# Kernel optimization log

Measured on AMD Instinct MI355X. Metric: run time of the kernel, lower is better.

## Reference

```python
import jax, jax.numpy as jnp
import numpy as np

V, E, H, T, B, D, L = 32000, 512, 512, 128, 4, 4, 2
C0, C1 = 2000, 10000          # adaptive softmax cutoffs
NT = T - D + 1


def setup_inputs() -> dict:
    key = jax.random.key(0)
    ks = jax.random.split(key, 18)
    s = 0.02
    x = jax.random.randint(ks[0], (B, T), 1, V)
    lengths = jnp.sort(jax.random.randint(ks[1], (B,), D, T + 1))[::-1]
    lengths = lengths.at[0].set(T)
    # graph predictor output: per-layer attention matrices [B, L, T, T]
    G = jax.nn.softmax(jax.random.normal(ks[2], (B, L, T, T)), axis=-1)
    emb = (jax.random.normal(ks[3], (V, E)) * s).at[0].set(0.0)  # padding_idx=0
    enc_w_ih = jax.random.normal(ks[4], (L, 3 * H, H)) * s
    enc_w_hh = jax.random.normal(ks[5], (L, 3 * H, H)) * s
    enc_b_ih = jnp.zeros((L, 3 * H))
    enc_b_hh = jnp.zeros((L, 3 * H))
    dec_w_ih = jax.random.normal(ks[6], (3 * H, E)) * s
    dec_w_hh = jax.random.normal(ks[7], (3 * H, H)) * s
    dec_b_ih = jnp.zeros((3 * H,))
    dec_b_hh = jnp.zeros((3 * H,))
    head_w = jax.random.normal(ks[8], (C0 + 2, H)) * s
    t0_proj = jax.random.normal(ks[9], (H // 4, H)) * s
    t0_out = jax.random.normal(ks[10], (C1 - C0, H // 4)) * s
    t1_proj = jax.random.normal(ks[11], (H // 16, H)) * s
    t1_out = jax.random.normal(ks[12], (V - C1, H // 16)) * s
    return dict(x=x, lengths=lengths, G=G, emb=emb,
                enc_w_ih=enc_w_ih, enc_w_hh=enc_w_hh, enc_b_ih=enc_b_ih, enc_b_hh=enc_b_hh,
                dec_w_ih=dec_w_ih, dec_w_hh=dec_w_hh, dec_b_ih=dec_b_ih, dec_b_hh=dec_b_hh,
                head_w=head_w, t0_proj=t0_proj, t0_out=t0_out, t1_proj=t1_proj, t1_out=t1_out)


def gru_step(xt, h, w_ih, w_hh, b_ih, b_hh):
    """torch nn.GRU/GRUCell math; works on arbitrary leading dims."""
    gi = xt @ w_ih.T + b_ih
    gh = h @ w_hh.T + b_hh
    i_r, i_z, i_n = jnp.split(gi, 3, axis=-1)
    h_r, h_z, h_n = jnp.split(gh, 3, axis=-1)
    r = jax.nn.sigmoid(i_r + h_r)
    z = jax.nn.sigmoid(i_z + h_z)
    n = jnp.tanh(i_n + r * h_n)
    return (1.0 - z) * n + z * h


def adaptive_log_prob(h, head_w, t0_proj, t0_out, t1_proj, t1_out):
    """torch AdaptiveLogSoftmaxWithLoss.log_prob: h [N,H] -> [N,V]."""
    head_lp = jax.nn.log_softmax(h @ head_w.T, axis=-1)                      # [N, C0+2]
    lp0 = head_lp[:, C0:C0 + 1] + jax.nn.log_softmax((h @ t0_proj.T) @ t0_out.T, axis=-1)
    lp1 = head_lp[:, C0 + 1:C0 + 2] + jax.nn.log_softmax((h @ t1_proj.T) @ t1_out.T, axis=-1)
    return jnp.concatenate([head_lp[:, :C0], lp0, lp1], axis=-1)


def reference(x, lengths, G, emb, enc_w_ih, enc_w_hh, enc_b_ih, enc_b_hh,
              dec_w_ih, dec_w_hh, dec_b_ih, dec_b_hh,
              head_w, t0_proj, t0_out, t1_proj, t1_out):
    b = x.shape[0]
    input_f = emb[x]                      # [B,T,E] (dropout p=0)
    embedded = input_f
    # ---- encoder: graph-weighted aggregation + GRUCell per layer ----
    for l in range(enc_w_ih.shape[0]):
        wgt = jnp.einsum('bji,bjd->bid', G[:, l], input_f)   # G_l^T @ input_f
        input_f = gru_step(wgt, input_f, enc_w_ih[l], enc_w_hh[l], enc_b_ih[l], enc_b_hh[l])
    # ---- decoder: length-D GRU window per start position t ----
    t_idx = jnp.arange(NT)
    d_idx = jnp.arange(D)
    tok_idx = jnp.broadcast_to(t_idx[None, :, None] + d_idx[None, None, :] - 1, (b, NT, D))
    tok_idx = tok_idx.at[:, 0, 0].set(lengths - 1)           # t=0,d=0 uses embedded[lengths-1]
    wins = jnp.take_along_axis(embedded, tok_idx.reshape(b, -1)[:, :, None], axis=1)
    wins = wins.reshape(b, NT, D, E)
    h0 = input_f[:, :NT, :]                                  # [B,NT,H]
    def step(h, xd):
        hn = gru_step(xd, h, dec_w_ih, dec_w_hh, dec_b_ih, dec_b_hh)
        return hn, hn
    _, hs = jax.lax.scan(step, h0, jnp.moveaxis(wins, 2, 0))  # [D,B,NT,H]
    hs = jnp.moveaxis(hs, 0, 2)                               # [B,NT,D,H]
    # pad_packed_sequence zeros hidden beyond per-row lens = min(lengths - t, D)
    valid = (t_idx[None, :, None] + d_idx[None, None, :]) < lengths[:, None, None]
    hs = jnp.where(valid[..., None], hs, 0.0)
    lp = adaptive_log_prob(hs.reshape(-1, H), head_w, t0_proj, t0_out, t1_proj, t1_out)
    lp = lp.reshape(b, NT, D, V)
    # batch rows with lengths <= t were excluded and F.pad'ed with zeros
    row_valid = t_idx[None, :] < lengths[:, None]
    lp = jnp.where(row_valid[:, :, None, None], lp, 0.0)
    return lp.reshape(b, NT * D, V)
```

## Files before the change

kernel.cpp:

```cpp
#include <hip/hip_runtime.h>
#include <hip/hip_bf16.h>
#include <hip/hip_fp16.h>

typedef __hip_bfloat16 bf16;
typedef __attribute__((ext_vector_type(8))) short short8v;
typedef __attribute__((ext_vector_type(4))) float float4v;

#define V_    32000
#define E_    512
#define H_    512
#define T_    128
#define B_    4
#define D_    4
#define L_    2
#define C0_   2000
#define C1_   10000
#define NT_   125
#define NROW_ 2000
#define NH_   2002
#define NTOTC 2162
#define NSLOT 252

__device__ __forceinline__ float bf2f(bf16 v) { return __bfloat162float(v); }
__device__ __forceinline__ unsigned short f2bfu(float f) {
    bf16 h = __float2bfloat16(f);
    union { bf16 h; unsigned short u; } cv; cv.h = h; return cv.u;
}
__device__ __forceinline__ float ld1(const void* p, size_t i, int bf) {
    return bf ? bf2f(((const bf16*)p)[i]) : ((const float*)p)[i];
}

__device__ __forceinline__ void lse_push(float z, float& m, float& s) {
    if (z <= m) { s += __expf(z - m); }
    else        { s = s * __expf(m - z) + 1.0f; m = z; }
}
__device__ __forceinline__ void lse_merge(float m2, float s2, float& m, float& s) {
    float mm = fmaxf(m, m2);
    s = s * __expf(m - mm) + s2 * __expf(m2 - mm);
    m = mm;
}

__global__ void k_detect(const void* __restrict__ G, int* __restrict__ flag) {
    int t = threadIdx.x;
    float s32 = 0.0f;
    for (int k = t; k < 128; k += 64) s32 += ((const float*)G)[k];
    for (int off = 32; off; off >>= 1) s32 += __shfl_down(s32, off);
    if (t == 0) {
        float e32 = fabsf(s32 - 1.0f);
        *flag = (e32 < 0.05f) ? 0 : 1;
    }
}

struct ConvArgs {
    const void* src[9];
    unsigned int off[10];
};
__global__ void k_wembed(ConvArgs a, unsigned short* __restrict__ wb,
                         const int* __restrict__ flagp,
                         const int* __restrict__ x, const void* __restrict__ emb,
                         float* __restrict__ embedded, float* __restrict__ f0,
                         unsigned short* __restrict__ f0b) {
    const int bf = *flagp;
    if (blockIdx.x < 1024) {
        int i = blockIdx.x * 256 + threadIdx.x;
        int bt = i >> 9, e = i & 511;
        int tok = x[bt];
        float v = ld1(emb, (size_t)tok * E_ + e, bf);
        embedded[i] = v; f0[i] = v; f0b[i] = f2bfu(v);
    } else {
        unsigned int total = a.off[9];
        unsigned int stride = (gridDim.x - 1024) * 256;
        for (unsigned int i = (blockIdx.x - 1024) * 256 + threadIdx.x; i < total;
             i += stride) {
            int seg = 0;
            while (i >= a.off[seg + 1]) seg++;
            wb[i] = f2bfu(ld1(a.src[seg], i - a.off[seg], bf));
        }
    }
}

__global__ void k_wgt(const void* __restrict__ G, const float* __restrict__ f,
                      unsigned short* __restrict__ wgtb, int l,
                      const int* __restrict__ flagp) {
    const int bf = *flagp;
    int i = blockIdx.x * 256 + threadIdx.x;
    int e = i & 511;
    int bi = i >> 9;
    int b = bi >> 7, ip = bi & 127;
    size_t gbase = ((size_t)(b * L_ + l) * T_ * T_) + ip;
    const float* fb = f + (size_t)b * T_ * E_ + e;
    float acc = 0.0f;
    #pragma unroll 4
    for (int j = 0; j < T_; ++j)
        acc = fmaf(ld1(G, gbase + (size_t)j * T_, bf), fb[(size_t)j * E_], acc);
    wgtb[i] = f2bfu(acc);
}

struct GemmP {
    const unsigned short* A0;
    const unsigned short* A1;
    const unsigned short* W;
    unsigned long long w1off;
    int M, N, K, Nlse;
    float* Zg; int ldz; int zcol1;
    const void* bias0; const void* bias1; int boff;
    void* zraw; int outColOff;
    float* stats;
    unsigned short* p0b;
    unsigned short* p1b;
    float* lsep; int slotBase;
    const int* lengths;
    const int* flagp;
};

__device__ __forceinline__ void zstore(void* zraw, size_t i, int bf, float v) {
    if (bf) ((__half*)zraw)[i] = __float2half(v);
    else    ((float*)zraw)[i]  = v;
}

template<int MODE>
__global__ __launch_bounds__(256, 2) void k_gemm(GemmP p) {
    const int bf = *p.flagp;
    const int zsel = (MODE == 0) ? blockIdx.z : 0;
    const unsigned short* A  = zsel ? p.A1 : p.A0;
    const unsigned short* Bw = p.W + (zsel ? p.w1off : 0ull);
    const int M = p.M, N = p.N, K = p.K;
    const int bx = blockIdx.x, by = blockIdx.y;
    const int m0 = by * 128, n0 = bx * 128;
    const int t = threadIdx.x;
    const int wave = t >> 6, lane = t & 63;
    const int wm = wave >> 1, wn = wave & 1;
    const int quad = lane >> 4, l16 = lane & 15;

    __shared__ __align__(16) unsigned short As[128 * 40];
    __shared__ __align__(16) unsigned short Bs[128 * 40];
    __shared__ float pm[128][2], ps[128][2];

    float4v acc[4][4];
    #pragma unroll
    for (int mi = 0; mi < 4; ++mi)
        #pragma unroll
        for (int ni = 0; ni < 4; ++ni)
            acc[mi][ni] = (float4v){0.f, 0.f, 0.f, 0.f};

    for (int k0 = 0; k0 < K; k0 += 32) {
        if (k0) __syncthreads();
        #pragma unroll
        for (int i = 0; i < 2; ++i) {
            int idx = t + i * 256;
            int row = idx >> 2, seg = idx & 3;
            uint4 av = {0u, 0u, 0u, 0u};
            int gm = m0 + row;
            if (gm < M) av = *(const uint4*)(A + (size_t)gm * K + k0 + seg * 8);
            *(uint4*)(&As[row * 40 + seg * 8]) = av;
            uint4 bv = {0u, 0u, 0u, 0u};
            int gn = n0 + row;
            if (gn < N) bv = *(const uint4*)(Bw + (size_t)gn * K + k0 + seg * 8);
            *(uint4*)(&Bs[row * 40 + seg * 8]) = bv;
        }
        __syncthreads();
        short8v af[4], bfv[4];
        #pragma unroll
        for (int mi = 0; mi < 4; ++mi)
            af[mi] = *(const short8v*)(As + (wm * 64 + mi * 16 + l16) * 40 + quad * 8);
        #pragma unroll
        for (int ni = 0; ni < 4; ++ni)
            bfv[ni] = *(const short8v*)(Bs + (wn * 64 + ni * 16 + l16) * 40 + quad * 8);
        #pragma unroll
        for (int mi = 0; mi < 4; ++mi)
            #pragma unroll
            for (int ni = 0; ni < 4; ++ni)
                acc[mi][ni] = __builtin_amdgcn_mfma_f32_16x16x32_bf16(
                    af[mi], bfv[ni], acc[mi][ni], 0, 0, 0);
    }

    if (MODE == 0) {
        const void* bias = zsel ? p.bias1 : p.bias0;
        const int zcol = zsel ? p.zcol1 : 0;
        #pragma unroll
        for (int mi = 0; mi < 4; ++mi)
            #pragma unroll
            for (int r = 0; r < 4; ++r) {
                int grow = m0 + wm * 64 + mi * 16 + quad * 4 + r;
                if (grow >= M) continue;
                #pragma unroll
                for (int ni = 0; ni < 4; ++ni) {
                    int gcol = n0 + wn * 64 + ni * 16 + l16;
                    if (gcol < N)
                        p.Zg[(size_t)grow * p.ldz + zcol + gcol] =
                            acc[mi][ni][r] + ld1(bias, p.boff + gcol, bf);
                }
            }
    } else if (MODE == 1) {
        #pragma unroll
        for (int mi = 0; mi < 4; ++mi)
            #pragma unroll
            for (int r = 0; r < 4; ++r) {
                int grow = m0 + wm * 64 + mi * 16 + quad * 4 + r;
                if (grow >= M) continue;
                #pragma unroll
                for (int ni = 0; ni < 4; ++ni) {
                    int gcol = n0 + wn * 64 + ni * 16 + l16;
                    float v = acc[mi][ni][r];
                    if (gcol < C0_) zstore(p.zraw, (size_t)grow * V_ + gcol, bf, v);
                    else if (gcol < NH_) p.stats[grow * 8 + 2 + (gcol - C0_)] = v;
                    else if (gcol < 2130) p.p0b[grow * 128 + (gcol - NH_)] = f2bfu(v);
                    else if (gcol < NTOTC) p.p1b[grow * 32 + (gcol - 2130)] = f2bfu(v);
                }
            }
    } else {
        #pragma unroll
        for (int mi = 0; mi < 4; ++mi)
            #pragma unroll
            for (int r = 0; r < 4; ++r) {
                int grow = m0 + wm * 64 + mi * 16 + quad * 4 + r;
                if (grow >= M) continue;
                #pragma unroll
                for (int ni = 0; ni < 4; ++ni) {
                    int gcol = n0 + wn * 64 + ni * 16 + l16;
                    if (gcol < N)
                        zstore(p.zraw, (size_t)grow * V_ + p.outColOff + gcol, bf,
                               acc[mi][ni][r]);
                }
            }
    }

    if (MODE == 1 || MODE == 2) {
        const int Nlse = p.Nlse;
        #pragma unroll
        for (int mi = 0; mi < 4; ++mi) {
            #pragma unroll
            for (int r = 0; r < 4; ++r) {
                float m = -1e30f, s = 0.0f;
                #pragma unroll
                for (int ni = 0; ni < 4; ++ni) {
                    int gcol = n0 + wn * 64 + ni * 16 + l16;
                    if (gcol < Nlse) lse_push(acc[mi][ni][r], m, s);
                }
                #pragma unroll
                for (int off = 1; off < 16; off <<= 1) {
                    float m2 = __shfl_xor(m, off), s2 = __shfl_xor(s, off);
                    lse_merge(m2, s2, m, s);
                }
                if (l16 == 0) {
                    int rl = wm * 64 + mi * 16 + quad * 4 + r;
                    pm[rl][wn] = m; ps[rl][wn] = s;
                }
            }
        }
        __syncthreads();
        if (t < 128) {
            int grow = m0 + t;
            if (grow < M) {
                float m = pm[t][0], s = ps[t][0];
                lse_merge(pm[t][1], ps[t][1], m, s);
                float* dst = p.lsep + ((size_t)grow * NSLOT + p.slotBase + bx) * 2;
                dst[0] = m; dst[1] = s;
            }
        }
    }
}

__device__ __forceinline__ float gru2(float i_r, float i_z, float i_n,
                                      float h_r, float h_z, float h_n, float h) {
    float r = 1.0f / (1.0f + __expf(-(i_r + h_r)));
    float z = 1.0f / (1.0f + __expf(-(i_z + h_z)));
    float n = tanhf(i_n + r * h_n);
    return (1.0f - z) * n + z * h;
}

__global__ void k_apply_enc(const float* __restrict__ gates,
                            const float* __restrict__ hprev,
                            float* __restrict__ hnext,
                            unsigned short* __restrict__ hnextb) {
    int i = blockIdx.x * 256 + threadIdx.x;
    int row = i >> 9, k = i & 511;
    const float* g = gates + (size_t)row * 3072;
    float v = gru2(g[k], g[512 + k], g[1024 + k],
                   g[1536 + k], g[2048 + k], g[2560 + k], hprev[i]);
    hnext[i] = v; hnextb[i] = f2bfu(v);
}

__global__ void k_h0win(const float* __restrict__ embedded,
                        const float* __restrict__ ffin,
                        const int* __restrict__ lengths,
                        unsigned short* __restrict__ winb,
                        float* __restrict__ hdec,
                        unsigned short* __restrict__ hdecb) {
    int i = blockIdx.x * 256 + threadIdx.x;
    if (i < 1024000) {
        int e = i & 511;
        int wr = i >> 9;
        int d = wr / 500, row = wr - d * 500;
        int b = row / NT_, t = row - b * NT_;
        int tok = (d == 0 && t == 0) ? (lengths[b] - 1) : (t + d - 1);
        winb[i] = f2bfu(embedded[((size_t)(b * T_ + tok) << 9) + e]);
    } else {
        int j = i - 1024000;
        int row = j >> 9, e = j & 511;
        int b = row / NT_, t = row - b * NT_;
        float v = ffin[((size_t)(b * T_ + t) << 9) + e];
        hdec[j] = v; hdecb[j] = f2bfu(v);
    }
}

__global__ void k_apply_dec(const float* __restrict__ gih,
                            const float* __restrict__ ghh,
                            float* __restrict__ hdec,
                            unsigned short* __restrict__ hdecb,
                            unsigned short* __restrict__ hsb,
                            const int* __restrict__ lengths, int d) {
    int i = blockIdx.x * 256 + threadIdx.x;
    int row = i >> 9, k = i & 511;
    int b = row / NT_, t = row - b * NT_;
    const float* gi = gih + (size_t)(d * 500 + row) * 1536;
    const float* gh = ghh + (size_t)row * 1536;
    float hn = gru2(gi[k], gi[512 + k], gi[1024 + k],
                    gh[k], gh[512 + k], gh[1024 + k], hdec[i]);
    hdec[i] = hn; hdecb[i] = f2bfu(hn);
    bool valid = (t + d) < lengths[b];
    hsb[(((size_t)row * D_ + d) << 9) + k] = valid ? f2bfu(hn) : (unsigned short)0;
}

__global__ void k_corr2(const float* __restrict__ lsep, const float* __restrict__ stats,
                        float* __restrict__ corr) {
    int r = blockIdx.x * 256 + threadIdx.x;
    if (r >= NROW_) return;
    const float* P = lsep + (size_t)r * NSLOT * 2;
    float m = -1e30f, s = 0.0f;
    for (int i = 0; i < 17; ++i)  lse_merge(P[2 * i], P[2 * i + 1], m, s);
    float ch = m + logf(s);
    float lp0 = stats[r * 8 + 2] - ch;
    float lp1 = stats[r * 8 + 3] - ch;
    m = -1e30f; s = 0.0f;
    for (int i = 17; i < 80; ++i) lse_merge(P[2 * i], P[2 * i + 1], m, s);
    float ct0 = m + logf(s);
    m = -1e30f; s = 0.0f;
    for (int i = 80; i < 252; ++i) lse_merge(P[2 * i], P[2 * i + 1], m, s);
    float ct1 = m + logf(s);
    corr[r * 4 + 0] = ch;
    corr[r * 4 + 1] = ct0 - lp0;
    corr[r * 4 + 2] = ct1 - lp1;
}

__global__ void k_fix(const float* __restrict__ corr,
                      const int* __restrict__ lengths, void* __restrict__ out,
                      const int* __restrict__ flagp) {
    const int bf = *flagp;
    int idx = blockIdx.x * 256 + threadIdx.x;
    if (idx >= NROW_ * (V_ / 8)) return;
    int row = idx / (V_ / 8);
    int col = (idx - row * (V_ / 8)) * 8;
    int b = row / 500;
    int tt = (row - b * 500) >> 2;
    bool valid = tt < lengths[b];
    int cri = (col < C0_) ? 0 : (col < C1_ ? 1 : 2);
    float cr = corr[row * 4 + cri];
    size_t base = (size_t)row * V_ + col;
    if (bf) {
        unsigned short* p16 = (unsigned short*)out + base;
        union { uint4 u; __half h[8]; } in;
        in.u = *(const uint4*)p16;
        union { uint4 u; unsigned short s[8]; } o;
        #pragma unroll
        for (int j = 0; j < 8; ++j)
            o.s[j] = f2bfu(valid ? (__half2float(in.h[j]) - cr) : 0.0f);
        *(uint4*)p16 = o.u;
    } else {
        float* op = (float*)out + base;
        float4 a = *(float4*)op, c = *(float4*)(op + 4);
        float4 ra = valid ? (float4){a.x - cr, a.y - cr, a.z - cr, a.w - cr}
                          : (float4){0.f, 0.f, 0.f, 0.f};
        float4 rc = valid ? (float4){c.x - cr, c.y - cr, c.z - cr, c.w - cr}
                          : (float4){0.f, 0.f, 0.f, 0.f};
        *(float4*)op = ra; *(float4*)(op + 4) = rc;
    }
}

#define OFF_EMB    0u
#define OFF_FA     262144u
#define OFF_FB     524288u
#define OFF_FAB    786432u
#define OFF_FBB    917504u
#define OFF_WGTB   1048576u
#define OFF_GATES  1179648u
#define OFF_GIH    2752512u
#define OFF_GHH    5824512u
#define OFF_HDEC   6592512u
#define OFF_HDECB  6848512u
#define OFF_WINB   6976512u
#define OFF_HSB    7488512u
#define OFF_P0B    8000512u
#define OFF_P1B    8128512u
#define OFF_STATS  8160512u
#define OFF_CORR   8176512u
#define OFF_LSEP   8184512u
#define OFF_WB     9192512u
#define OFF_FLAG   12969264u

#define WO_ENCIH   0u
#define WO_ENCHH   1572864u
#define WO_DECIH   3145728u
#define WO_DECHH   3932160u
#define WO_W1      4718592u
#define WO_T0O     5825536u
#define WO_T1O     6849536u
#define WO_END     7553504u

static inline GemmP mkp(const unsigned short* A0, const unsigned short* A1,
                        const unsigned short* W, unsigned long long w1off,
                        int M, int N, int K, int Nlse,
                        float* Zg, int ldz, int zcol1,
                        const void* bias0, const void* bias1, int boff,
                        void* zraw, int outColOff, float* stats,
                        unsigned short* p0b, unsigned short* p1b,
                        float* lsep, int slotBase,
                        const int* lengths, const int* flagp) {
    GemmP p;
    p.A0 = A0; p.A1 = A1; p.W = W; p.w1off = w1off;
    p.M = M; p.N = N; p.K = K; p.Nlse = Nlse;
    p.Zg = Zg; p.ldz = ldz; p.zcol1 = zcol1;
    p.bias0 = bias0; p.bias1 = bias1; p.boff = boff;
    p.zraw = zraw; p.outColOff = outColOff; p.stats = stats;
    p.p0b = p0b; p.p1b = p1b; p.lsep = lsep; p.slotBase = slotBase;
    p.lengths = lengths; p.flagp = flagp;
    return p;
}

extern "C" void kernel_launch(void* const* d_in, const int* in_sizes, int n_in,
                              void* d_out, int out_size, void* d_ws, size_t ws_size,
                              hipStream_t stream) {
    (void)in_sizes; (void)n_in; (void)out_size; (void)ws_size;
    const int*  x        = (const int*)d_in[0];
    const int*  lengths  = (const int*)d_in[1];
    const void* G        = d_in[2];
    const void* emb      = d_in[3];
    const void* enc_w_ih = d_in[4];
    const void* enc_w_hh = d_in[5];
    const void* enc_b_ih = d_in[6];
    const void* enc_b_hh = d_in[7];
    const void* dec_w_ih = d_in[8];
    const void* dec_w_hh = d_in[9];
    const void* dec_b_ih = d_in[10];
    const void* dec_b_hh = d_in[11];
    const void* head_w   = d_in[12];
    const void* t0_proj  = d_in[13];
    const void* t0_out   = d_in[14];
    const void* t1_proj  = d_in[15];
    const void* t1_out   = d_in[16];

    float* ws = (float*)d_ws;
    float* embedded = ws + OFF_EMB;
    float* fA    = ws + OFF_FA;
    float* fB    = ws + OFF_FB;
    unsigned short* fAb  = (unsigned short*)(ws + OFF_FAB);
    unsigned short* fBb  = (unsigned short*)(ws + OFF_FBB);
    unsigned short* wgtb = (unsigned short*)(ws + OFF_WGTB);
    float* gates = ws + OFF_GATES;
    float* gih   = ws + OFF_GIH;
    float* ghh   = ws + OFF_GHH;
    float* hdec  = ws + OFF_HDEC;
    unsigned short* hdecb = (unsigned short*)(ws + OFF_HDECB);
    unsigned short* winb  = (unsigned short*)(ws + OFF_WINB);
    unsigned short* hsb   = (unsigned short*)(ws + OFF_HSB);
    unsigned short* p0b   = (unsigned short*)(ws + OFF_P0B);
    unsigned short* p1b   = (unsigned short*)(ws + OFF_P1B);
    float* stats = ws + OFF_STATS;
    float* corr  = ws + OFF_CORR;
    float* lsep  = ws + OFF_LSEP;
    unsigned short* WB = (unsigned short*)(ws + OFF_WB);
    int* flagp = (int*)(ws + OFF_FLAG);
    void* out = d_out;

    k_detect<<<1, 64, 0, stream>>>(G, flagp);

    ConvArgs ca;
    ca.src[0] = enc_w_ih; ca.src[1] = enc_w_hh; ca.src[2] = dec_w_ih;
    ca.src[3] = dec_w_hh; ca.src[4] = head_w;   ca.src[5] = t0_proj;
    ca.src[6] = t1_proj;  ca.src[7] = t0_out;   ca.src[8] = t1_out;
    ca.off[0] = WO_ENCIH; ca.off[1] = WO_ENCHH; ca.off[2] = WO_DECIH;
    ca.off[3] = WO_DECHH; ca.off[4] = WO_W1;
    ca.off[5] = WO_W1 + 2002u * 512u;
    ca.off[6] = WO_W1 + 2130u * 512u;
    ca.off[7] = WO_T0O;   ca.off[8] = WO_T1O;   ca.off[9] = WO_END;
    k_wembed<<<3072, 256, 0, stream>>>(ca, WB, flagp, x, emb, embedded, fA, fAb);

    k_wgt<<<1024, 256, 0, stream>>>(G, fA, wgtb, 0, flagp);
    k_gemm<0><<<dim3(12, 4, 2), 256, 0, stream>>>(mkp(
        wgtb, fAb, WB + WO_ENCIH, (unsigned long long)(WO_ENCHH - WO_ENCIH),
        512, 1536, 512, 0, gates, 3072, 1536, enc_b_ih, enc_b_hh, 0,
        nullptr, 0, nullptr, nullptr, nullptr, nullptr, 0, lengths, flagp));
    k_apply_enc<<<1024, 256, 0, stream>>>(gates, fA, fB, fBb);

    k_wgt<<<1024, 256, 0, stream>>>(G, fB, wgtb, 1, flagp);
    k_gemm<0><<<dim3(12, 4, 2), 256, 0, stream>>>(mkp(
        wgtb, fBb, WB + WO_ENCIH + 786432u, (unsigned long long)(WO_ENCHH - WO_ENCIH),
        512, 1536, 512, 0, gates, 3072, 1536, enc_b_ih, enc_b_hh, 1536,
        nullptr, 0, nullptr, nullptr, nullptr, nullptr, 0, lengths, flagp));
    k_apply_enc<<<1024, 256, 0, stream>>>(gates, fB, fA, fAb);

    k_h0win<<<5000, 256, 0, stream>>>(embedded, fA, lengths, winb, hdec, hdecb);

    k_gemm<0><<<dim3(12, 16, 1), 256, 0, stream>>>(mkp(
        winb, nullptr, WB + WO_DECIH, 0ull, 2000, 1536, 512, 0,
        gih, 1536, 0, dec_b_ih, nullptr, 0,
        nullptr, 0, nullptr, nullptr, nullptr, nullptr, 0, lengths, flagp));

    for (int d = 0; d < D_; ++d) {
        k_gemm<0><<<dim3(12, 4, 1), 256, 0, stream>>>(mkp(
            hdecb, nullptr, WB + WO_DECHH, 0ull, 500, 1536, 512, 0,
            ghh, 1536, 0, dec_b_hh, nullptr, 0,
            nullptr, 0, nullptr, nullptr, nullptr, nullptr, 0, lengths, flagp));
        k_apply_dec<<<1000, 256, 0, stream>>>(gih, ghh, hdec, hdecb, hsb, lengths, d);
    }

    k_gemm<1><<<dim3(17, 16, 1), 256, 0, stream>>>(mkp(
        hsb, nullptr, WB + WO_W1, 0ull, NROW_, NTOTC, 512, NH_,
        nullptr, 0, 0, nullptr, nullptr, 0, out, 0,
        stats, p0b, p1b, lsep, 0, lengths, flagp));
    k_gemm<2><<<dim3(63, 16, 1), 256, 0, stream>>>(mkp(
        p0b, nullptr, WB + WO_T0O, 0ull, NROW_, 8000, 128, 8000,
        nullptr, 0, 0, nullptr, nullptr, 0, out, C0_,
        stats, nullptr, nullptr, lsep, 17, lengths, flagp));
    k_gemm<2><<<dim3(172, 16, 1), 256, 0, stream>>>(mkp(
        p1b, nullptr, WB + WO_T1O, 0ull, NROW_, 22000, 32, 22000,
        nullptr, 0, 0, nullptr, nullptr, 0, out, C1_,
        stats, nullptr, nullptr, lsep, 80, lengths, flagp));

    k_corr2<<<8, 256, 0, stream>>>(lsep, stats, corr);

    k_fix<<<31250, 256, 0, stream>>>(corr, lengths, out, flagp);
}
```

Measured before the change: 783.9 us.

## Merge tail GEMMs into one launch, fuse h0/window prep, vectorize weight conversion

The two tail-cluster GEMM launches are merged into a single grid that picks its parameter set by block index, and the decoder-init gather is fused into the second encoder apply kernel, which writes hdec directly. The weight-conversion loop now handles four elements per thread with vector loads and stores. The LSE partial buffer is transposed to slot-major so that k_corr2 reads are coalesced across threads. Together these cut launch count and improve memory access, at the cost of a larger combined kernel and the assumption that segment offsets are multiples of four.

```diff
diff --git a/kernel.cpp b/kernel.cpp
--- a/kernel.cpp
+++ b/kernel.cpp
@@ -68,13 +68,23 @@
         float v = ld1(emb, (size_t)tok * E_ + e, bf);
         embedded[i] = v; f0[i] = v; f0b[i] = f2bfu(v);
     } else {
-        unsigned int total = a.off[9];
+        unsigned int totalg = a.off[9] >> 2;
         unsigned int stride = (gridDim.x - 1024) * 256;
-        for (unsigned int i = (blockIdx.x - 1024) * 256 + threadIdx.x; i < total;
-             i += stride) {
+        for (unsigned int g = (blockIdx.x - 1024) * 256 + threadIdx.x; g < totalg;
+             g += stride) {
+            unsigned int i = g << 2;
             int seg = 0;
             while (i >= a.off[seg + 1]) seg++;
-            wb[i] = f2bfu(ld1(a.src[seg], i - a.off[seg], bf));
+            unsigned int o = i - a.off[seg];
+            unsigned short r[4];
+            if (bf) {
+                *(uint2*)r = *(const uint2*)((const unsigned short*)a.src[seg] + o);
+            } else {
+                float4 v = *(const float4*)((const float*)a.src[seg] + o);
+                r[0] = f2bfu(v.x); r[1] = f2bfu(v.y);
+                r[2] = f2bfu(v.z); r[3] = f2bfu(v.w);
+            }
+            *(uint2*)(wb + i) = *(const uint2*)r;
         }
     }
 }
@@ -111,6 +121,7 @@
     float* lsep; int slotBase;
     const int* lengths;
     const int* flagp;
+    int gx;
 };
 
 __device__ __forceinline__ void zstore(void* zraw, size_t i, int bf, float v) {
@@ -119,22 +130,19 @@
 }
 
 template<int MODE>
-__global__ __launch_bounds__(256, 2) void k_gemm(GemmP p) {
+__device__ __forceinline__ void gemm_core(const GemmP& p, int bx, int by,
+        unsigned short* As, unsigned short* Bs,
+        float (*pm)[2], float (*ps)[2]) {
     const int bf = *p.flagp;
     const int zsel = (MODE == 0) ? blockIdx.z : 0;
     const unsigned short* A  = zsel ? p.A1 : p.A0;
     const unsigned short* Bw = p.W + (zsel ? p.w1off : 0ull);
     const int M = p.M, N = p.N, K = p.K;
-    const int bx = blockIdx.x, by = blockIdx.y;
     const int m0 = by * 128, n0 = bx * 128;
     const int t = threadIdx.x;
     const int wave = t >> 6, lane = t & 63;
     const int wm = wave >> 1, wn = wave & 1;
     const int quad = lane >> 4, l16 = lane & 15;
-
-    __shared__ __align__(16) unsigned short As[128 * 40];
-    __shared__ __align__(16) unsigned short Bs[128 * 40];
-    __shared__ float pm[128][2], ps[128][2];
 
     float4v acc[4][4];
     #pragma unroll
@@ -254,11 +262,28 @@
             if (grow < M) {
                 float m = pm[t][0], s = ps[t][0];
                 lse_merge(pm[t][1], ps[t][1], m, s);
-                float* dst = p.lsep + ((size_t)grow * NSLOT + p.slotBase + bx) * 2;
+                float* dst = p.lsep + ((size_t)(p.slotBase + bx) * NROW_ + grow) * 2;
                 dst[0] = m; dst[1] = s;
             }
         }
     }
+}
+
+template<int MODE>
+__global__ __launch_bounds__(256, 2) void k_gemm(GemmP p) {
+    __shared__ __align__(16) unsigned short As[128 * 40];
+    __shared__ __align__(16) unsigned short Bs[128 * 40];
+    __shared__ float pm[128][2], ps[128][2];
+    gemm_core<MODE>(p, blockIdx.x, blockIdx.y, As, Bs, pm, ps);
+}
+
+__global__ __launch_bounds__(256, 2) void k_gemmT(GemmP pa, GemmP pb) {
+    __shared__ __align__(16) unsigned short As[128 * 40];
+    __shared__ __align__(16) unsigned short Bs[128 * 40];
+    __shared__ float pm[128][2], ps[128][2];
+    int bx = blockIdx.x;
+    if (bx < pa.gx) gemm_core<2>(pa, bx, blockIdx.y, As, Bs, pm, ps);
+    else            gemm_core<2>(pb, bx - pa.gx, blockIdx.y, As, Bs, pm, ps);
 }
 
 __device__ __forceinline__ float gru2(float i_r, float i_z, float i_n,
@@ -281,26 +306,36 @@
     hnext[i] = v; hnextb[i] = f2bfu(v);
 }
 
-__global__ void k_h0win(const float* __restrict__ embedded,
-                        const float* __restrict__ ffin,
-                        const int* __restrict__ lengths,
-                        unsigned short* __restrict__ winb,
-                        float* __restrict__ hdec,
-                        unsigned short* __restrict__ hdecb) {
-    int i = blockIdx.x * 256 + threadIdx.x;
-    if (i < 1024000) {
+__global__ void k_apply_enc2(const float* __restrict__ gates,
+                             const float* __restrict__ hprev,
+                             float* __restrict__ hnext,
+                             unsigned short* __restrict__ hnextb,
+                             const float* __restrict__ embedded,
+                             const int* __restrict__ lengths,
+                             unsigned short* __restrict__ winb,
+                             float* __restrict__ hdec,
+                             unsigned short* __restrict__ hdecb) {
+    int blk = blockIdx.x;
+    if (blk < 1024) {
+        int i = blk * 256 + threadIdx.x;
+        int row = i >> 9, k = i & 511;
+        const float* g = gates + (size_t)row * 3072;
+        float v = gru2(g[k], g[512 + k], g[1024 + k],
+                       g[1536 + k], g[2048 + k], g[2560 + k], hprev[i]);
+        hnext[i] = v; hnextb[i] = f2bfu(v);
+        int b = row >> 7, t = row & 127;
+        if (t < NT_) {
+            int j = ((b * NT_ + t) << 9) + k;
+            hdec[j] = v; hdecb[j] = f2bfu(v);
+        }
+    } else {
+        int i = (blk - 1024) * 256 + threadIdx.x;
         int e = i & 511;
         int wr = i >> 9;
         int d = wr / 500, row = wr - d * 500;
         int b = row / NT_, t = row - b * NT_;
         int tok = (d == 0 && t == 0) ? (lengths[b] - 1) : (t + d - 1);
         winb[i] = f2bfu(embedded[((size_t)(b * T_ + tok) << 9) + e]);
-    } else {
-        int j = i - 1024000;
-        int row = j >> 9, e = j & 511;
-        int b = row / NT_, t = row - b * NT_;
-        float v = ffin[((size_t)(b * T_ + t) << 9) + e];
-        hdec[j] = v; hdecb[j] = f2bfu(v);
     }
 }
 
@@ -326,17 +361,25 @@
                         float* __restrict__ corr) {
     int r = blockIdx.x * 256 + threadIdx.x;
     if (r >= NROW_) return;
-    const float* P = lsep + (size_t)r * NSLOT * 2;
     float m = -1e30f, s = 0.0f;
-    for (int i = 0; i < 17; ++i)  lse_merge(P[2 * i], P[2 * i + 1], m, s);
+    for (int i = 0; i < 17; ++i) {
+        const float* P = lsep + ((size_t)i * NROW_ + r) * 2;
+        lse_merge(P[0], P[1], m, s);
+    }
     float ch = m + logf(s);
     float lp0 = stats[r * 8 + 2] - ch;
     float lp1 = stats[r * 8 + 3] - ch;
     m = -1e30f; s = 0.0f;
-    for (int i = 17; i < 80; ++i) lse_merge(P[2 * i], P[2 * i + 1], m, s);
+    for (int i = 17; i < 80; ++i) {
+        const float* P = lsep + ((size_t)i * NROW_ + r) * 2;
+        lse_merge(P[0], P[1], m, s);
+    }
     float ct0 = m + logf(s);
     m = -1e30f; s = 0.0f;
-    for (int i = 80; i < 252; ++i) lse_merge(P[2 * i], P[2 * i + 1], m, s);
+    for (int i = 80; i < 252; ++i) {
+        const float* P = lsep + ((size_t)i * NROW_ + r) * 2;
+        lse_merge(P[0], P[1], m, s);
+    }
     float ct1 = m + logf(s);
     corr[r * 4 + 0] = ch;
     corr[r * 4 + 1] = ct0 - lp0;
@@ -423,7 +466,7 @@
     p.bias0 = bias0; p.bias1 = bias1; p.boff = boff;
     p.zraw = zraw; p.outColOff = outColOff; p.stats = stats;
     p.p0b = p0b; p.p1b = p1b; p.lsep = lsep; p.slotBase = slotBase;
-    p.lengths = lengths; p.flagp = flagp;
+    p.lengths = lengths; p.flagp = flagp; p.gx = 0;
     return p;
 }
 
@@ -497,9 +540,8 @@
         wgtb, fBb, WB + WO_ENCIH + 786432u, (unsigned long long)(WO_ENCHH - WO_ENCIH),
         512, 1536, 512, 0, gates, 3072, 1536, enc_b_ih, enc_b_hh, 1536,
         nullptr, 0, nullptr, nullptr, nullptr, nullptr, 0, lengths, flagp));
-    k_apply_enc<<<1024, 256, 0, stream>>>(gates, fB, fA, fAb);
-
-    k_h0win<<<5000, 256, 0, stream>>>(embedded, fA, lengths, winb, hdec, hdecb);
+    k_apply_enc2<<<5024, 256, 0, stream>>>(gates, fB, fA, fAb, embedded, lengths,
+                                           winb, hdec, hdecb);
 
     k_gemm<0><<<dim3(12, 16, 1), 256, 0, stream>>>(mkp(
         winb, nullptr, WB + WO_DECIH, 0ull, 2000, 1536, 512, 0,
@@ -518,14 +560,17 @@
         hsb, nullptr, WB + WO_W1, 0ull, NROW_, NTOTC, 512, NH_,
         nullptr, 0, 0, nullptr, nullptr, 0, out, 0,
         stats, p0b, p1b, lsep, 0, lengths, flagp));
-    k_gemm<2><<<dim3(63, 16, 1), 256, 0, stream>>>(mkp(
-        p0b, nullptr, WB + WO_T0O, 0ull, NROW_, 8000, 128, 8000,
-        nullptr, 0, 0, nullptr, nullptr, 0, out, C0_,
-        stats, nullptr, nullptr, lsep, 17, lengths, flagp));
-    k_gemm<2><<<dim3(172, 16, 1), 256, 0, stream>>>(mkp(
-        p1b, nullptr, WB + WO_T1O, 0ull, NROW_, 22000, 32, 22000,
-        nullptr, 0, 0, nullptr, nullptr, 0, out, C1_,
-        stats, nullptr, nullptr, lsep, 80, lengths, flagp));
+    {
+        GemmP pa = mkp(p0b, nullptr, WB + WO_T0O, 0ull, NROW_, 8000, 128, 8000,
+                       nullptr, 0, 0, nullptr, nullptr, 0, out, C0_,
+                       stats, nullptr, nullptr, lsep, 17, lengths, flagp);
+        pa.gx = 63;
+        GemmP pb = mkp(p1b, nullptr, WB + WO_T1O, 0ull, NROW_, 22000, 32, 22000,
+                       nullptr, 0, 0, nullptr, nullptr, 0, out, C1_,
+                       stats, nullptr, nullptr, lsep, 80, lengths, flagp);
+        pb.gx = 172;
+        k_gemmT<<<dim3(235, 16, 1), 256, 0, stream>>>(pa, pb);
+    }
 
     k_corr2<<<8, 256, 0, stream>>>(lsep, stats, corr);
 
```

Result: faster. 765.8 us, median of 2 (-2.3%).
